# Kernel tuning notes

Measured on AMD Instinct MI355X. Metric: run time of the kernel, lower is better.

The kernel has to match this reference:

```python
import jax, jax.numpy as jnp
import numpy as np

R_HEADS = 4   # read heads
CELL = 64     # cell_size (word width)
MEM = 512     # nr_cells
DELTA = 1e-6


def _content_weights(mem, keys, strengths):
    # mem: (B,M,Wc), keys: (B,K,Wc), strengths: (B,K) -> (B,K,M)
    mn = jnp.linalg.norm(mem, axis=2, keepdims=True) + DELTA
    kn = jnp.linalg.norm(keys, axis=2, keepdims=True) + DELTA
    d = jnp.einsum('bkw,bmw->bkm', keys / kn, mem / mn)  # cosine similarity
    return jax.nn.softmax(d * strengths[:, :, None], axis=2)


def _allocate(usage):
    # usage: (B,M) -> allocation weighting (B,M)
    B = usage.shape[0]
    u = DELTA + (1.0 - DELTA) * usage
    idx = jnp.argsort(u, axis=1)                               # ascending usage
    sorted_u = jnp.take_along_axis(u, idx, axis=1)
    prod_su = jnp.cumprod(
        jnp.concatenate([jnp.ones((B, 1), u.dtype), sorted_u], axis=1), axis=1)[:, :-1]
    sorted_alloc = (1.0 - sorted_u) * prod_su
    inv = jnp.argsort(idx, axis=1)                             # inverse permutation
    return jnp.take_along_axis(sorted_alloc, inv, axis=1)


def dnc_forward(x, W_ih, b_ih, W_hh, b_hh, W_out, b_out, W_int, b_int, W_mem, b_mem):
    B, T, IN = x.shape
    H = W_hh.shape[1]
    r, w, m = R_HEADS, CELL, MEM
    eye_mask = 1.0 - jnp.eye(m, dtype=x.dtype)  # zero link-matrix diagonal

    def step(carry, x_t):
        h, c, mem, link, prec, read_w, write_w, usage, last_read = carry
        # controller LSTM cell (torch gate order i,f,g,o)
        inp = jnp.concatenate([x_t, last_read], axis=1)
        gates = inp @ W_ih.T + b_ih + h @ W_hh.T + b_hh
        gi, gf, gg, go = jnp.split(gates, 4, axis=1)
        c = jax.nn.sigmoid(gf) * c + jax.nn.sigmoid(gi) * jnp.tanh(gg)
        h = jax.nn.sigmoid(go) * jnp.tanh(c)
        out = h @ W_out.T + b_out
        xi = h @ W_int.T + b_int  # interface vector, size r*w+3w+5r+3
        # parse interface
        o = r * w
        read_keys = jnp.tanh(xi[:, :r * w].reshape(B, r, w))
        read_str = jax.nn.softplus(xi[:, o:o + r]); o += r
        write_key = jnp.tanh(xi[:, o:o + w].reshape(B, 1, w)); o += w
        write_str = jax.nn.softplus(xi[:, o:o + 1]); o += 1
        erase = jax.nn.sigmoid(xi[:, o:o + w].reshape(B, 1, w)); o += w
        write_vec = jnp.tanh(xi[:, o:o + w].reshape(B, 1, w)); o += w
        free_gates = jax.nn.sigmoid(xi[:, o:o + r]); o += r
        alloc_gate = jax.nn.sigmoid(xi[:, o:o + 1]); o += 1
        write_gate = jax.nn.sigmoid(xi[:, o:o + 1]); o += 1
        read_modes = jax.nn.softmax(xi[:, o:o + 3 * r].reshape(B, r, 3), axis=-1)

        # ---- write ----
        usage = usage + (1 - usage) * (1 - jnp.prod(1 - write_w, axis=1))
        psi = jnp.prod(1 - free_gates[:, :, None] * read_w, axis=1)
        usage = usage * psi
        wcw = _content_weights(mem, write_key, write_str)      # (B,1,M)
        alloc = _allocate(usage)[:, None, :]                   # (B,1,M)
        ag = alloc_gate[:, :, None]
        write_w = write_gate[:, :, None] * (ag * alloc + (1 - ag) * wcw)
        reset = jnp.prod(1 - write_w[:, :, :, None] * erase[:, :, None, :], axis=1)  # (B,M,Wc)
        mem = mem * reset + jnp.einsum('bkm,bkw->bmw', write_w, write_vec)
        ww = write_w[:, 0]                                     # (B,M), single write head
        L = link[:, 0]
        L = (1 - ww[:, :, None] - ww[:, None, :]) * L + ww[:, :, None] * prec[:, 0][:, None, :]
        L = L * eye_mask
        link = L[:, None]
        prec = (1 - jnp.sum(write_w, axis=2, keepdims=True)) * prec + write_w

        # ---- read ----
        cw = _content_weights(mem, read_keys, read_str)        # (B,R,M)
        fwd = jnp.einsum('bij,brj->bri', L, read_w)
        bwd = jnp.einsum('bri,bij->brj', read_w, L)
        read_w = (read_modes[:, :, 0:1] * bwd
                  + read_modes[:, :, 1:2] * fwd
                  + read_modes[:, :, 2:3] * cw)
        read_vecs = jnp.einsum('brm,bmw->brw', read_w, mem).reshape(B, r * w)
        y = jnp.concatenate([out, read_vecs], axis=1) @ W_mem.T + b_mem
        return (h, c, mem, link, prec, read_w, write_w, usage, read_vecs), y

    z = lambda *s: jnp.zeros(s, x.dtype)
    carry0 = (z(B, H), z(B, H), z(B, m, w), z(B, 1, m, m), z(B, 1, m),
              z(B, r, m), z(B, 1, m), z(B, m), z(B, r * w))
    _, ys = jax.lax.scan(step, carry0, jnp.swapaxes(x, 0, 1))
    return jnp.swapaxes(ys, 0, 1)  # (B,T,IN)


def setup_inputs() -> dict:
    key = jax.random.key(0)
    ks = jax.random.split(key, 12)
    B, T, IN, H = 16, 32, 256, 512
    r, w = R_HEADS, CELL
    iface = w * r + 3 * w + 5 * r + 3  # 471
    s = 0.05
    return {
        'x': jax.random.normal(ks[0], (B, T, IN), jnp.float32),
        'W_ih': jax.random.normal(ks[1], (4 * H, IN + r * w), jnp.float32) * s,
        'b_ih': jax.random.normal(ks[2], (4 * H,), jnp.float32) * s,
        'W_hh': jax.random.normal(ks[3], (4 * H, H), jnp.float32) * s,
        'b_hh': jax.random.normal(ks[4], (4 * H,), jnp.float32) * s,
        'W_out': jax.random.normal(ks[5], (H, H), jnp.float32) * s,
        'b_out': jax.random.normal(ks[6], (H,), jnp.float32) * s,
        'W_int': jax.random.normal(ks[7], (iface, H), jnp.float32) * s,
        'b_int': jax.random.normal(ks[8], (iface,), jnp.float32) * s,
        'W_mem': jax.random.normal(ks[9], (IN, r * w + H), jnp.float32) * s,
        'b_mem': jax.random.normal(ks[10], (IN,), jnp.float32) * s,
    }


def reference(x, W_ih, b_ih, W_hh, b_hh, W_out, b_out, W_int, b_int, W_mem, b_mem):
    return dnc_forward(x, W_ih, b_ih, W_hh, b_hh, W_out, b_out, W_int, b_int, W_mem, b_mem)
```

## Files before the change

### kernel.cpp

```cpp
#include <hip/hip_runtime.h>
#include <math.h>

#define NB 16
#define NT 256
#define NWG 256
#define TT 32
#define INP 256
#define HH 512
#define RH 4
#define CWID 64
#define MM 512
#define IFACE 471
#define DELTA 1e-6f
#define AP 516

__device__ __align__(16) float g_h[2][NB][HH];
__device__ __align__(16) float g_c[NB][HH];
__device__ __align__(16) float g_lr[NB][INP];
__device__ __align__(16) float g_usage[NB][MM];
__device__ __align__(16) float g_ww[NB][MM];
__device__ __align__(16) float g_prec[2][NB][MM];
__device__ __align__(16) float g_rw[NB][RH][MM];
__device__ __align__(16) float g_mem[NB][MM][CWID];
__device__ __align__(16) float g_L[NB][MM][MM];
__device__ __align__(16) float g_out[NB][HH];
__device__ __align__(16) float g_xi[NB][HH];
__device__ __align__(16) float g_rkn[NB][RH][CWID];
__device__ __align__(16) float g_rs[NB][RH];
__device__ __align__(16) float g_erase[NB][CWID];
__device__ __align__(16) float g_wv[NB][CWID];
__device__ __align__(16) float g_modes[NB][RH][3];
__device__ __align__(16) float g_fwd[NB][RH][MM];
__device__ __align__(16) float g_bwdp[NB][16][RH][MM];
__device__ __align__(16) float g_e[NB][RH][MM];
__device__ __align__(16) float g_cwsp[NB][16][RH];
__device__ __align__(16) float g_rvp[NB][16][RH][CWID];

struct P {
  const float *x, *W_ih, *b_ih, *W_hh, *b_hh, *W_out, *b_out, *W_int, *b_int, *W_mem, *b_mem;
  float* y;
};

__device__ __forceinline__ float sigf(float x)  { return 1.f / (1.f + __expf(-x)); }
__device__ __forceinline__ float splus(float x) { return fmaxf(x, 0.f) + log1pf(__expf(-fabsf(x))); }

__device__ __forceinline__ void zfill(float* a, long n) {
  const long stride = (long)gridDim.x * blockDim.x;
  for (long i = (long)blockIdx.x * blockDim.x + threadIdx.x; i < n; i += stride) a[i] = 0.f;
}

__global__ void __launch_bounds__(NT) k_init() {
  zfill(&g_h[0][0][0], 2L*NB*HH);
  zfill(&g_c[0][0], (long)NB*HH);
  zfill(&g_lr[0][0], (long)NB*INP);
  zfill(&g_usage[0][0], (long)NB*MM);
  zfill(&g_ww[0][0], (long)NB*MM);
  zfill(&g_prec[0][0][0], 2L*NB*MM);
  zfill(&g_rw[0][0][0], (long)NB*RH*MM);
  zfill(&g_mem[0][0][0], (long)NB*MM*CWID);
  zfill(&g_L[0][0][0], (long)NB*MM*MM);
}

__global__ void __launch_bounds__(NT) k_ph1(P p, int t) {
  __shared__ __align__(16) float sm[14432];
  float* As  = sm;
  float* Ws  = sm + 16*AP;
  float* red = sm + 24*AP;
  const int tid = threadIdx.x;
  const int j0  = 2 * (int)blockIdx.x;
  const int op  = tid & 3;
  const int bq  = (tid >> 2) & 3;
  const int ks  = tid >> 4;
  const float (*hsrc)[HH] = g_h[t & 1];
  float acc0[4] = {0.f,0.f,0.f,0.f};
  float acc1[4] = {0.f,0.f,0.f,0.f};
  for (int pass = 0; pass < 2; ++pass) {
    if (pass == 0) {
      for (int idx = tid; idx < NB*INP; idx += NT) {
        int b = idx >> 8, k = idx & 255;
        As[b*AP + k] = p.x[((size_t)b*TT + t)*INP + k];
      }
      for (int idx = tid; idx < NB*INP; idx += NT) {
        int b = idx >> 8, k = idx & 255;
        As[b*AP + INP + k] = g_lr[b][k];
      }
    } else {
      for (int idx = tid; idx < NB*HH; idx += NT) {
        int b = idx >> 9, k = idx & 511;
        As[b*AP + k] = hsrc[b][k];
      }
    }
    const float* Wsrc = pass ? p.W_hh : p.W_ih;
    for (int idx = tid; idx < 8*512; idx += NT) {
      int ro = idx >> 9, k = idx & 511;
      int row = (ro >> 1)*HH + j0 + (ro & 1);
      Ws[ro*AP + k] = Wsrc[(size_t)row*512 + k];
    }
    __syncthreads();
    const int k0 = ks * 32;
    #pragma unroll
    for (int k4 = 0; k4 < 32; k4 += 4) {
      const float4 w0 = *(const float4*)&Ws[(op*2+0)*AP + k0 + k4];
      const float4 w1 = *(const float4*)&Ws[(op*2+1)*AP + k0 + k4];
      #pragma unroll
      for (int bb = 0; bb < 4; ++bb) {
        const float4 a = *(const float4*)&As[(bq*4+bb)*AP + k0 + k4];
        acc0[bb] += a.x*w0.x + a.y*w0.y + a.z*w0.z + a.w*w0.w;
        acc1[bb] += a.x*w1.x + a.y*w1.y + a.z*w1.z + a.w*w1.w;
      }
    }
    __syncthreads();
  }
  #pragma unroll
  for (int bb = 0; bb < 4; ++bb) {
    red[(op*2+0)*256 + (bq*4+bb)*16 + ks] = acc0[bb];
    red[(op*2+1)*256 + (bq*4+bb)*16 + ks] = acc1[bb];
  }
  __syncthreads();
  if (tid < 128) {
    int o = tid >> 4, b = tid & 15;
    float s = 0.f;
    #pragma unroll
    for (int q = 0; q < 16; ++q) s += red[o*256 + b*16 + q];
    int row = (o >> 1)*HH + j0 + (o & 1);
    red[o*256 + b*16] = s + p.b_ih[row] + p.b_hh[row];
  }
  __syncthreads();
  if (tid < 32) {
    int jj = tid >> 4, b = tid & 15;
    int j  = j0 + jj;
    float gi = red[(0+jj)*256 + b*16];
    float gf = red[(2+jj)*256 + b*16];
    float gg = red[(4+jj)*256 + b*16];
    float go = red[(6+jj)*256 + b*16];
    float c0 = g_c[b][j];
    float cn = sigf(gf)*c0 + sigf(gi)*tanhf(gg);
    float hn = sigf(go)*tanhf(cn);
    g_c[b][j] = cn;
    g_h[(t+1) & 1][b][j] = hn;
  }
}

__global__ void __launch_bounds__(NT) k_ph2(P p, int t) {
  __shared__ __align__(16) float sm[10576];
  float* hs  = sm;
  float* Ws  = sm + 16*AP;
  float* red = sm + 20*AP;
  const int tid = threadIdx.x;
  const int o0  = 4 * (int)blockIdx.x;
  const float (*hcur)[HH] = g_h[(t+1) & 1];
  for (int idx = tid; idx < NB*HH; idx += NT) {
    int b = idx >> 9, k = idx & 511;
    hs[b*AP + k] = hcur[b][k];
  }
  for (int idx = tid; idx < 4*512; idx += NT) {
    int oi = idx >> 9, k = idx & 511;
    int o = o0 + oi;
    float v = 0.f;
    if (o < HH)              v = p.W_out[(size_t)o*512 + k];
    else if (o < HH + IFACE) v = p.W_int[(size_t)(o - HH)*512 + k];
    Ws[oi*AP + k] = v;
  }
  __syncthreads();
  {
    const int b = tid & 15, oi = (tid >> 4) & 3, ks = tid >> 6;
    const int k0 = ks * 128;
    float acc = 0.f;
    #pragma unroll 8
    for (int k4 = 0; k4 < 128; k4 += 4) {
      const float4 a  = *(const float4*)&hs[b*AP + k0 + k4];
      const float4 wv = *(const float4*)&Ws[oi*AP + k0 + k4];
      acc += a.x*wv.x + a.y*wv.y + a.z*wv.z + a.w*wv.w;
    }
    red[(oi*16 + b)*4 + ks] = acc;
  }
  __syncthreads();
  if (tid < 64) {
    int oi = tid >> 4, b = tid & 15;
    int base = (oi*16 + b)*4;
    float s = red[base] + red[base+1] + red[base+2] + red[base+3];
    int o = o0 + oi;
    if (o < HH) g_out[b][o] = s + p.b_out[o];
    else if (o < HH + IFACE) g_xi[b][o - HH] = s + p.b_int[o - HH];
  }
}

__global__ void __launch_bounds__(512) k_ph3(int pp) {
  __shared__ __align__(16) float sm[4152];
  const int b = (int)blockIdx.x, tid = threadIdx.x;
  float* xi_l = sm;
  float* wkn  = sm + 472;
  float* sc   = sm + 536;
  float* u_l  = sm + 552;
  float* wcw  = sm + 1064;
  float* su   = sm + 1576;
  float* cB   = sm + 2600;
  float* wwl  = sm + 3112;
  float* red  = sm + 3624;
  int*   rnk  = (int*)(sm + 3640);

  for (int i = tid; i < IFACE; i += 512) xi_l[i] = g_xi[b][i];
  __syncthreads();
  {
    const int wv = tid >> 6, v = tid & 63;
    if (wv < 4) {
      float kv = tanhf(xi_l[wv*64 + v]);
      float ss = kv * kv;
      #pragma unroll
      for (int d = 1; d < 64; d <<= 1) ss += __shfl_xor(ss, d, 64);
      g_rkn[b][wv][v] = kv / (sqrtf(ss) + DELTA);
      if (v == 0) { float s_ = splus(xi_l[256 + wv]); sc[wv] = s_; g_rs[b][wv] = s_; }
    } else if (wv == 4) {
      float kv = tanhf(xi_l[260 + v]);
      float ss = kv * kv;
      #pragma unroll
      for (int d = 1; d < 64; d <<= 1) ss += __shfl_xor(ss, d, 64);
      wkn[v] = kv / (sqrtf(ss) + DELTA);
    } else if (wv == 5) {
      g_erase[b][v] = sigf(xi_l[325 + v]);
    } else if (wv == 6) {
      g_wv[b][v] = tanhf(xi_l[389 + v]);
    } else {
      if (v < 4)       sc[4 + v] = sigf(xi_l[453 + v]);
      else if (v == 4) sc[8] = sigf(xi_l[457]);
      else if (v == 5) sc[9] = sigf(xi_l[458]);
      else if (v == 6) sc[10] = splus(xi_l[324]);
      else if (v >= 8 && v < 12) {
        int r = v - 8;
        float a0 = xi_l[459 + r*3], a1 = xi_l[459 + r*3 + 1], a2 = xi_l[459 + r*3 + 2];
        float mx = fmaxf(a0, fmaxf(a1, a2));
        float e0 = __expf(a0 - mx), e1 = __expf(a1 - mx), e2 = __expf(a2 - mx);
        float si = e0 + e1 + e2;
        g_modes[b][r][0] = e0/si; g_modes[b][r][1] = e1/si; g_modes[b][r][2] = e2/si;
      }
    }
  }
  __syncthreads();
  {
    float uo = g_usage[b][tid];
    float wwp = g_ww[b][tid];
    float psi = 1.f;
    #pragma unroll
    for (int r = 0; r < RH; ++r) psi *= 1.f - sc[4+r]*g_rw[b][r][tid];
    float un = (uo + (1.f - uo)*wwp) * psi;
    g_usage[b][tid] = un;
    u_l[tid] = DELTA + (1.f - DELTA)*un;
  }
  {
    float dot = 0.f, nn = 0.f;
    const float* mr = &g_mem[b][tid][0];
    #pragma unroll
    for (int v4 = 0; v4 < CWID; v4 += 4) {
      float4 m4 = *(const float4*)&mr[v4];
      dot += m4.x*wkn[v4] + m4.y*wkn[v4+1] + m4.z*wkn[v4+2] + m4.w*wkn[v4+3];
      nn  += m4.x*m4.x + m4.y*m4.y + m4.z*m4.z + m4.w*m4.w;
    }
    wcw[tid] = (dot / (sqrtf(nn) + DELTA)) * sc[10];
  }
  __syncthreads();
  {
    const int wv = tid >> 6, v = tid & 63;
    float x0 = wcw[tid];
    float mx = x0;
    #pragma unroll
    for (int d = 1; d < 64; d <<= 1) mx = fmaxf(mx, __shfl_xor(mx, d, 64));
    if (v == 0) red[wv] = mx;
    __syncthreads();
    float gmx = red[0];
    #pragma unroll
    for (int q = 1; q < 8; ++q) gmx = fmaxf(gmx, red[q]);
    float e0 = __expf(x0 - gmx);
    float ss = e0;
    #pragma unroll
    for (int d = 1; d < 64; d <<= 1) ss += __shfl_xor(ss, d, 64);
    if (v == 0) red[8 + wv] = ss;
    __syncthreads();
    float tot = red[8];
    #pragma unroll
    for (int q = 9; q < 16; ++q) tot += red[q];
    wcw[tid] = e0 / tot;
  }
  __syncthreads();
  {
    const float u0 = u_l[tid];
    int cnt = 0;
    for (int j = 0; j < MM; j += 8) {
      const float4 a = *(const float4*)&u_l[j];
      const float4 c = *(const float4*)&u_l[j + 4];
      cnt += (a.x < u0) || (a.x == u0 && (j+0) < tid);
      cnt += (a.y < u0) || (a.y == u0 && (j+1) < tid);
      cnt += (a.z < u0) || (a.z == u0 && (j+2) < tid);
      cnt += (a.w < u0) || (a.w == u0 && (j+3) < tid);
      cnt += (c.x < u0) || (c.x == u0 && (j+4) < tid);
      cnt += (c.y < u0) || (c.y == u0 && (j+5) < tid);
      cnt += (c.z < u0) || (c.z == u0 && (j+6) < tid);
      cnt += (c.w < u0) || (c.w == u0 && (j+7) < tid);
    }
    rnk[tid] = cnt;
    su[cnt] = u0;
  }
  __syncthreads();
  {
    const int lane = tid & 63, wv = tid >> 6;
    float v = su[tid];
    #pragma unroll
    for (int d = 1; d < 64; d <<= 1) {
      float m = __shfl_up(v, d, 64);
      if (lane >= d) v *= m;
    }
    if (lane == 63) red[wv] = v;
    __syncthreads();
    float pre = 1.f;
    for (int q = 0; q < wv; ++q) pre *= red[q];
    cB[tid] = v * pre;
    __syncthreads();
    float ag = sc[8], wgt = sc[9];
    int rk = rnk[tid];
    float excl = rk ? cB[rk - 1] : 1.f;
    float alloc = (1.f - u_l[tid]) * excl;
    float wn = wgt * (ag*alloc + (1.f - ag)*wcw[tid]);
    wwl[tid] = wn;
    g_ww[b][tid] = wn;
  }
  __syncthreads();
  {
    const int wv = tid >> 6, v = tid & 63;
    float s2 = wwl[tid];
    #pragma unroll
    for (int d = 1; d < 64; d <<= 1) s2 += __shfl_xor(s2, d, 64);
    if (v == 0) red[wv] = s2;
    __syncthreads();
    float sww = red[0];
    #pragma unroll
    for (int q = 1; q < 8; ++q) sww += red[q];
    g_prec[1 - pp][b][tid] = (1.f - sww)*g_prec[pp][b][tid] + wwl[tid];
  }
}

__global__ void __launch_bounds__(NT) k_ph4(int pp) {
  __shared__ __align__(16) float sm[6608];
  const int w = (int)blockIdx.x, tid = threadIdx.x;
  const int b = w >> 4, s = w & 15, i0 = s * 32;
  float* pl   = sm;
  float* wwl  = sm + 512;
  float* rwl  = sm + 1024;
  float* el   = sm + 3072;
  float* wvl  = sm + 3136;
  float* rknl = sm + 3200;
  float* rs4  = sm + 3456;
  float* fp   = sm + 3472;
  float* mt   = sm + 4496;
  float* nrm  = sm + 6576;

  for (int i = tid; i < MM; i += NT) { pl[i] = g_prec[pp][b][i]; wwl[i] = g_ww[b][i]; }
  for (int i = tid; i < RH*MM; i += NT) rwl[i] = g_rw[b][i >> 9][i & 511];
  for (int i = tid; i < CWID; i += NT) { el[i] = g_erase[b][i]; wvl[i] = g_wv[b][i]; }
  for (int i = tid; i < RH*CWID; i += NT) rknl[i] = g_rkn[b][i >> 6][i & 63];
  if (tid < 4) rs4[tid] = g_rs[b][tid];
  __syncthreads();
  {
    const int ii = tid >> 3, js = tid & 7;
    const int i = i0 + ii;
    const float wwi = wwl[i];
    float f0=0.f, f1=0.f, f2=0.f, f3=0.f;
    float* Lrow = &g_L[b][i][0];
    #pragma unroll
    for (int step = 0; step < 16; ++step) {
      const int col = js*64 + ((js*8 + step*4) & 63);
      float4 l4 = *(float4*)&Lrow[col];
      float lv[4] = {l4.x, l4.y, l4.z, l4.w};
      #pragma unroll
      for (int q = 0; q < 4; ++q) {
        const int jq = col + q;
        float lnv = (1.f - wwi - wwl[jq]) * lv[q] + wwi * pl[jq];
        if (jq == i) lnv = 0.f;
        lv[q] = lnv;
        f0 += lnv * rwl[jq];
        f1 += lnv * rwl[512 + jq];
        f2 += lnv * rwl[1024 + jq];
        f3 += lnv * rwl[1536 + jq];
      }
      *(float4*)&Lrow[col] = make_float4(lv[0], lv[1], lv[2], lv[3]);
    }
    fp[(ii*8 + js)*4 + 0] = f0;
    fp[(ii*8 + js)*4 + 1] = f1;
    fp[(ii*8 + js)*4 + 2] = f2;
    fp[(ii*8 + js)*4 + 3] = f3;
  }
  __syncthreads();
  if (tid < 128) {
    int ii = tid >> 2, r = tid & 3;
    float sY = 0.f;
    #pragma unroll
    for (int js = 0; js < 8; ++js) sY += fp[(ii*8 + js)*4 + r];
    g_fwd[b][r][i0 + ii] = sY;
  }
  {
    const int j = tid * 2;
    float a00=0,a01=0,a10=0,a11=0,a20=0,a21=0,a30=0,a31=0;
    #pragma unroll 4
    for (int ii2 = 0; ii2 < 32; ++ii2) {
      const int i = i0 + ii2;
      const float2 l2 = *(const float2*)&g_L[b][i][j];
      const float r0 = rwl[i], r1 = rwl[512+i], r2 = rwl[1024+i], r3 = rwl[1536+i];
      a00 += r0*l2.x; a01 += r0*l2.y;
      a10 += r1*l2.x; a11 += r1*l2.y;
      a20 += r2*l2.x; a21 += r2*l2.y;
      a30 += r3*l2.x; a31 += r3*l2.y;
    }
    g_bwdp[b][s][0][j] = a00; g_bwdp[b][s][0][j+1] = a01;
    g_bwdp[b][s][1][j] = a10; g_bwdp[b][s][1][j+1] = a11;
    g_bwdp[b][s][2][j] = a20; g_bwdp[b][s][2][j+1] = a21;
    g_bwdp[b][s][3][j] = a30; g_bwdp[b][s][3][j+1] = a31;
  }
  for (int idx = tid; idx < 32*CWID; idx += NT) {
    int ii = idx >> 6, v = idx & 63;
    int i = i0 + ii;
    float wwi = wwl[i];
    float mv = g_mem[b][i][v];
    float mn = mv * (1.f - wwi*el[v]) + wwi*wvl[v];
    g_mem[b][i][v] = mn;
    mt[ii*65 + v] = mn;
  }
  __syncthreads();
  {
    int ii = tid >> 3, js = tid & 7;
    float nn = 0.f;
    #pragma unroll
    for (int q = 0; q < 8; ++q) { float mv = mt[ii*65 + js*8 + q]; nn += mv*mv; }
    fp[(ii*8 + js)*4] = nn;
  }
  __syncthreads();
  if (tid < 32) {
    float nn = 0.f;
    #pragma unroll
    for (int q = 0; q < 8; ++q) nn += fp[(tid*8 + q)*4];
    nrm[tid] = sqrtf(nn) + DELTA;
  }
  __syncthreads();
  {
    int ii = tid >> 3, js = tid & 7;
    float p0=0,p1=0,p2=0,p3=0;
    #pragma unroll
    for (int q = 0; q < 8; ++q) {
      float mv = mt[ii*65 + js*8 + q];
      p0 += mv * rknl[ 0 + js*8 + q];
      p1 += mv * rknl[ 64 + js*8 + q];
      p2 += mv * rknl[128 + js*8 + q];
      p3 += mv * rknl[192 + js*8 + q];
    }
    fp[(ii*8 + js)*4 + 0] = p0;
    fp[(ii*8 + js)*4 + 1] = p1;
    fp[(ii*8 + js)*4 + 2] = p2;
    fp[(ii*8 + js)*4 + 3] = p3;
  }
  __syncthreads();
  if (tid < 128) {
    int ii = tid >> 2, r = tid & 3;
    float d = 0.f;
    #pragma unroll
    for (int js = 0; js < 8; ++js) d += fp[(ii*8 + js)*4 + r];
    float e = __expf((d / nrm[ii]) * rs4[r]);
    g_e[b][r][i0 + ii] = e;
    mt[ii*4 + r] = e;
  }
  __syncthreads();
  if (tid < 4) {
    float ssum = 0.f;
    #pragma unroll
    for (int q = 0; q < 32; ++q) ssum += mt[q*4 + tid];
    g_cwsp[b][s][tid] = ssum;
  }
}

__global__ void __launch_bounds__(NT) k_ph5() {
  __shared__ __align__(16) float sm[144];
  const int w = (int)blockIdx.x, tid = threadIdx.x;
  const int b = w >> 4, s = w & 15, j0 = s * 32;
  float* Sr  = sm;
  float* rwt = sm + 16;
  if (tid < 4) {
    float ss = 0.f;
    #pragma unroll
    for (int q = 0; q < 16; ++q) ss += g_cwsp[b][q][tid];
    Sr[tid] = ss;
  }
  __syncthreads();
  if (tid < 128) {
    int jj = tid >> 2, r = tid & 3;
    int j = j0 + jj;
    float bw = 0.f;
    #pragma unroll
    for (int q = 0; q < 16; ++q) bw += g_bwdp[b][q][r][j];
    float fw = g_fwd[b][r][j];
    float cwv = g_e[b][r][j] / Sr[r];
    float rn = g_modes[b][r][0]*bw + g_modes[b][r][1]*fw + g_modes[b][r][2]*cwv;
    g_rw[b][r][j] = rn;
    rwt[r*32 + jj] = rn;
  }
  __syncthreads();
  {
    int r = tid >> 6, v = tid & 63;
    float acc = 0.f;
    #pragma unroll
    for (int jj = 0; jj < 32; ++jj) acc += rwt[r*32 + jj] * g_mem[b][j0 + jj][v];
    g_rvp[b][s][r][v] = acc;
  }
}

__global__ void __launch_bounds__(NT) k_ph6(P p, int t) {
  __shared__ __align__(16) float sm[1024];
  const int w = (int)blockIdx.x, tid = threadIdx.x;
  const int b = w >> 4, s = w & 15, o0 = s * 16;
  float* rv   = sm;
  float* outl = sm + 256;
  float* red  = sm + 768;
  {
    int r = tid >> 6, v = tid & 63;
    float acc = 0.f;
    #pragma unroll
    for (int q = 0; q < 16; ++q) acc += g_rvp[b][q][r][v];
    rv[r*64 + v] = acc;
    if (s == 0) g_lr[b][r*64 + v] = acc;
  }
  for (int k = tid; k < HH; k += NT) outl[k] = g_out[b][k];
  __syncthreads();
  {
    int oi = tid & 15, ks = tid >> 4;
    int o = o0 + oi;
    const float* wm = &p.W_mem[(size_t)o * 768];
    float acc = 0.f;
    for (int k = ks*48; k < ks*48 + 48; ++k) {
      float a = (k < HH) ? outl[k] : rv[k - HH];
      acc += a * wm[k];
    }
    red[oi*16 + ks] = acc;
  }
  __syncthreads();
  if (tid < 16) {
    int o = o0 + tid;
    float ss = 0.f;
    #pragma unroll
    for (int q = 0; q < 16; ++q) ss += red[tid*16 + q];
    p.y[((size_t)b*TT + t)*INP + o] = ss + p.b_mem[o];
  }
}

extern "C" void kernel_launch(void* const* d_in, const int* in_sizes, int n_in,
                              void* d_out, int out_size, void* d_ws, size_t ws_size,
                              hipStream_t stream) {
  (void)in_sizes; (void)n_in; (void)out_size; (void)d_ws; (void)ws_size;
  P p;
  p.x     = (const float*)d_in[0];
  p.W_ih  = (const float*)d_in[1];
  p.b_ih  = (const float*)d_in[2];
  p.W_hh  = (const float*)d_in[3];
  p.b_hh  = (const float*)d_in[4];
  p.W_out = (const float*)d_in[5];
  p.b_out = (const float*)d_in[6];
  p.W_int = (const float*)d_in[7];
  p.b_int = (const float*)d_in[8];
  p.W_mem = (const float*)d_in[9];
  p.b_mem = (const float*)d_in[10];
  p.y     = (float*)d_out;

  k_init<<<dim3(1024), dim3(NT), 0, stream>>>();
  for (int t = 0; t < TT; ++t) {
    const int pp = t & 1;
    k_ph1<<<dim3(NWG), dim3(NT), 0, stream>>>(p, t);
    k_ph2<<<dim3(NWG), dim3(NT), 0, stream>>>(p, t);
    k_ph3<<<dim3(NB),  dim3(512), 0, stream>>>(pp);
    k_ph4<<<dim3(NWG), dim3(NT), 0, stream>>>(pp);
    k_ph5<<<dim3(NWG), dim3(NT), 0, stream>>>();
    k_ph6<<<dim3(NWG), dim3(NT), 0, stream>>>(p, t);
  }
}
```

Measured before the change: 2.162 ms.

## Hoist output projections out of the recurrent loop into batched post-loop kernels

The output projection (W_out on h) and the final y projection (W_mem on out and read vectors) are not on the recurrence path, so they move out of the per-timestep loop. Hidden states and per-slice read-vector partials are stored for every timestep, and two kernels run after the loop to compute all outputs at once, with weights held in shared memory. This removes one kernel launch per step and shrinks the ph2 grid to only the interface rows. In exchange it costs extra global buffers, and ph1 now sums the 16 read-vector partials itself.

```diff
diff --git a/kernel.cpp b/kernel.cpp
--- a/kernel.cpp
+++ b/kernel.cpp
@@ -13,17 +13,16 @@
 #define IFACE 471
 #define DELTA 1e-6f
 #define AP 516
+#define WMP 772
 
 __device__ __align__(16) float g_h[2][NB][HH];
 __device__ __align__(16) float g_c[NB][HH];
-__device__ __align__(16) float g_lr[NB][INP];
 __device__ __align__(16) float g_usage[NB][MM];
 __device__ __align__(16) float g_ww[NB][MM];
 __device__ __align__(16) float g_prec[2][NB][MM];
 __device__ __align__(16) float g_rw[NB][RH][MM];
 __device__ __align__(16) float g_mem[NB][MM][CWID];
 __device__ __align__(16) float g_L[NB][MM][MM];
-__device__ __align__(16) float g_out[NB][HH];
 __device__ __align__(16) float g_xi[NB][HH];
 __device__ __align__(16) float g_rkn[NB][RH][CWID];
 __device__ __align__(16) float g_rs[NB][RH];
@@ -34,7 +33,9 @@
 __device__ __align__(16) float g_bwdp[NB][16][RH][MM];
 __device__ __align__(16) float g_e[NB][RH][MM];
 __device__ __align__(16) float g_cwsp[NB][16][RH];
-__device__ __align__(16) float g_rvp[NB][16][RH][CWID];
+__device__ __align__(16) float g_hs[NB][TT][HH];
+__device__ __align__(16) float g_outs[NB][TT][HH];
+__device__ __align__(16) float g_rvps[NB][TT][16][RH*CWID];
 
 struct P {
   const float *x, *W_ih, *b_ih, *W_hh, *b_hh, *W_out, *b_out, *W_int, *b_int, *W_mem, *b_mem;
@@ -52,7 +53,6 @@
 __global__ void __launch_bounds__(NT) k_init() {
   zfill(&g_h[0][0][0], 2L*NB*HH);
   zfill(&g_c[0][0], (long)NB*HH);
-  zfill(&g_lr[0][0], (long)NB*INP);
   zfill(&g_usage[0][0], (long)NB*MM);
   zfill(&g_ww[0][0], (long)NB*MM);
   zfill(&g_prec[0][0][0], 2L*NB*MM);
@@ -82,7 +82,13 @@
       }
       for (int idx = tid; idx < NB*INP; idx += NT) {
         int b = idx >> 8, k = idx & 255;
-        As[b*AP + INP + k] = g_lr[b][k];
+        float s = 0.f;
+        if (t > 0) {
+          const float* rp = &g_rvps[b][t-1][0][k];
+          #pragma unroll
+          for (int q = 0; q < 16; ++q) s += rp[q*(RH*CWID)];
+        }
+        As[b*AP + INP + k] = s;
       }
     } else {
       for (int idx = tid; idx < NB*HH; idx += NT) {
@@ -138,6 +144,7 @@
     float hn = sigf(go)*tanhf(cn);
     g_c[b][j] = cn;
     g_h[(t+1) & 1][b][j] = hn;
+    g_hs[b][t][j] = hn;
   }
 }
 
@@ -156,10 +163,7 @@
   for (int idx = tid; idx < 4*512; idx += NT) {
     int oi = idx >> 9, k = idx & 511;
     int o = o0 + oi;
-    float v = 0.f;
-    if (o < HH)              v = p.W_out[(size_t)o*512 + k];
-    else if (o < HH + IFACE) v = p.W_int[(size_t)(o - HH)*512 + k];
-    Ws[oi*AP + k] = v;
+    Ws[oi*AP + k] = (o < IFACE) ? p.W_int[(size_t)o*512 + k] : 0.f;
   }
   __syncthreads();
   {
@@ -180,8 +184,7 @@
     int base = (oi*16 + b)*4;
     float s = red[base] + red[base+1] + red[base+2] + red[base+3];
     int o = o0 + oi;
-    if (o < HH) g_out[b][o] = s + p.b_out[o];
-    else if (o < HH + IFACE) g_xi[b][o - HH] = s + p.b_int[o - HH];
+    if (o < IFACE) g_xi[b][o] = s + p.b_int[o];
   }
 }
 
@@ -473,7 +476,7 @@
   }
 }
 
-__global__ void __launch_bounds__(NT) k_ph5() {
+__global__ void __launch_bounds__(NT) k_ph5(int t) {
   __shared__ __align__(16) float sm[144];
   const int w = (int)blockIdx.x, tid = threadIdx.x;
   const int b = w >> 4, s = w & 15, j0 = s * 32;
@@ -504,45 +507,92 @@
     float acc = 0.f;
     #pragma unroll
     for (int jj = 0; jj < 32; ++jj) acc += rwt[r*32 + jj] * g_mem[b][j0 + jj][v];
-    g_rvp[b][s][r][v] = acc;
-  }
-}
-
-__global__ void __launch_bounds__(NT) k_ph6(P p, int t) {
-  __shared__ __align__(16) float sm[1024];
+    g_rvps[b][t][s][tid] = acc;
+  }
+}
+
+__global__ void __launch_bounds__(NT) k_out_all(P p) {
+  __shared__ __align__(16) float sm[10576];
+  float* hs  = sm;
+  float* Ws  = sm + 16*AP;
+  float* red = sm + 20*AP;
+  const int tid = threadIdx.x;
+  const int wg  = (int)blockIdx.x & 127;
+  const int tg  = (int)blockIdx.x >> 7;
+  const int o0  = 4 * wg;
+  for (int idx = tid; idx < 4*512; idx += NT) {
+    int oi = idx >> 9, k = idx & 511;
+    Ws[oi*AP + k] = p.W_out[(size_t)(o0 + oi)*512 + k];
+  }
+  for (int tt = 0; tt < 16; ++tt) {
+    const int t = tg*16 + tt;
+    __syncthreads();
+    for (int idx = tid; idx < NB*HH; idx += NT) {
+      int b = idx >> 9, k = idx & 511;
+      hs[b*AP + k] = g_hs[b][t][k];
+    }
+    __syncthreads();
+    {
+      const int b = tid & 15, oi = (tid >> 4) & 3, ks = tid >> 6;
+      const int k0 = ks * 128;
+      float acc = 0.f;
+      #pragma unroll 8
+      for (int k4 = 0; k4 < 128; k4 += 4) {
+        const float4 a  = *(const float4*)&hs[b*AP + k0 + k4];
+        const float4 wv = *(const float4*)&Ws[oi*AP + k0 + k4];
+        acc += a.x*wv.x + a.y*wv.y + a.z*wv.z + a.w*wv.w;
+      }
+      red[(oi*16 + b)*4 + ks] = acc;
+    }
+    __syncthreads();
+    if (tid < 64) {
+      int oi = tid >> 4, b = tid & 15;
+      int base = (oi*16 + b)*4;
+      float s = red[base] + red[base+1] + red[base+2] + red[base+3];
+      g_outs[b][t][o0 + oi] = s + p.b_out[o0 + oi];
+    }
+  }
+}
+
+__global__ void __launch_bounds__(NT) k_y_all(P p) {
+  __shared__ __align__(16) float sm[16*WMP + 1024];
+  float* Wm   = sm;
+  float* outl = sm + 16*WMP;
+  float* rv   = sm + 16*WMP+512;
+  float* red  = sm + 16*WMP+768;
   const int w = (int)blockIdx.x, tid = threadIdx.x;
   const int b = w >> 4, s = w & 15, o0 = s * 16;
-  float* rv   = sm;
-  float* outl = sm + 256;
-  float* red  = sm + 768;
-  {
-    int r = tid >> 6, v = tid & 63;
-    float acc = 0.f;
-    #pragma unroll
-    for (int q = 0; q < 16; ++q) acc += g_rvp[b][q][r][v];
-    rv[r*64 + v] = acc;
-    if (s == 0) g_lr[b][r*64 + v] = acc;
-  }
-  for (int k = tid; k < HH; k += NT) outl[k] = g_out[b][k];
-  __syncthreads();
-  {
-    int oi = tid & 15, ks = tid >> 4;
-    int o = o0 + oi;
-    const float* wm = &p.W_mem[(size_t)o * 768];
-    float acc = 0.f;
-    for (int k = ks*48; k < ks*48 + 48; ++k) {
-      float a = (k < HH) ? outl[k] : rv[k - HH];
-      acc += a * wm[k];
-    }
-    red[oi*16 + ks] = acc;
-  }
-  __syncthreads();
-  if (tid < 16) {
-    int o = o0 + tid;
-    float ss = 0.f;
-    #pragma unroll
-    for (int q = 0; q < 16; ++q) ss += red[tid*16 + q];
-    p.y[((size_t)b*TT + t)*INP + o] = ss + p.b_mem[o];
+  for (int row = 0; row < 16; ++row)
+    for (int k = tid; k < 768; k += NT)
+      Wm[row*WMP + k] = p.W_mem[(size_t)(o0 + row)*768 + k];
+  for (int t = 0; t < TT; ++t) {
+    __syncthreads();
+    for (int k = tid; k < HH; k += NT) outl[k] = g_outs[b][t][k];
+    {
+      float acc = 0.f;
+      const float* rp = &g_rvps[b][t][0][tid];
+      #pragma unroll
+      for (int q = 0; q < 16; ++q) acc += rp[q*(RH*CWID)];
+      rv[tid] = acc;
+    }
+    __syncthreads();
+    {
+      int oi = tid & 15, ks = tid >> 4;
+      const float* wm = &Wm[oi*WMP];
+      float acc = 0.f;
+      for (int k = ks*48; k < ks*48 + 48; ++k) {
+        float a = (k < HH) ? outl[k] : rv[k - HH];
+        acc += a * wm[k];
+      }
+      red[oi*16 + ks] = acc;
+    }
+    __syncthreads();
+    if (tid < 16) {
+      float ss = 0.f;
+      #pragma unroll
+      for (int q = 0; q < 16; ++q) ss += red[tid*16 + q];
+      p.y[((size_t)b*TT + t)*INP + o0 + tid] = ss + p.b_mem[o0 + tid];
+    }
   }
 }
 
@@ -568,10 +618,11 @@
   for (int t = 0; t < TT; ++t) {
     const int pp = t & 1;
     k_ph1<<<dim3(NWG), dim3(NT), 0, stream>>>(p, t);
-    k_ph2<<<dim3(NWG), dim3(NT), 0, stream>>>(p, t);
+    k_ph2<<<dim3(118), dim3(NT), 0, stream>>>(p, t);
     k_ph3<<<dim3(NB),  dim3(512), 0, stream>>>(pp);
     k_ph4<<<dim3(NWG), dim3(NT), 0, stream>>>(pp);
-    k_ph5<<<dim3(NWG), dim3(NT), 0, stream>>>();
-    k_ph6<<<dim3(NWG), dim3(NT), 0, stream>>>(p, t);
-  }
-}
+    k_ph5<<<dim3(NWG), dim3(NT), 0, stream>>>(t);
+  }
+  k_out_all<<<dim3(256), dim3(NT), 0, stream>>>(p);
+  k_y_all<<<dim3(256), dim3(NT), 0, stream>>>(p);
+}
```

Result: slower. 2.304 ms (+6.6%).

## Move output projection off critical path into ph5 and skip link-matrix zero fill

Applied to the files above, without the earlier changes.

Phase 2 now computes only the interface vector (118 blocks instead of 256), and the W_out output projection moves into phase 5, where it runs beside the read-vector work. The aim is to shorten the serial chain leading into the memory-update phases. Separately, the 16 MB zero fill of the link matrix in init is removed, and phase 4 treats L as zero on the first timestep. In exchange, phase 5 takes on extra global weight reads per block and more shared memory.

```diff
diff --git a/kernel.cpp b/kernel.cpp
--- a/kernel.cpp
+++ b/kernel.cpp
@@ -58,7 +58,6 @@
   zfill(&g_prec[0][0][0], 2L*NB*MM);
   zfill(&g_rw[0][0][0], (long)NB*RH*MM);
   zfill(&g_mem[0][0][0], (long)NB*MM*CWID);
-  zfill(&g_L[0][0][0], (long)NB*MM*MM);
 }
 
 __global__ void __launch_bounds__(NT) k_ph1(P p, int t) {
@@ -156,10 +155,7 @@
   for (int idx = tid; idx < 4*512; idx += NT) {
     int oi = idx >> 9, k = idx & 511;
     int o = o0 + oi;
-    float v = 0.f;
-    if (o < HH)              v = p.W_out[(size_t)o*512 + k];
-    else if (o < HH + IFACE) v = p.W_int[(size_t)(o - HH)*512 + k];
-    Ws[oi*AP + k] = v;
+    Ws[oi*AP + k] = (o < IFACE) ? p.W_int[(size_t)o*512 + k] : 0.f;
   }
   __syncthreads();
   {
@@ -180,8 +176,7 @@
     int base = (oi*16 + b)*4;
     float s = red[base] + red[base+1] + red[base+2] + red[base+3];
     int o = o0 + oi;
-    if (o < HH) g_out[b][o] = s + p.b_out[o];
-    else if (o < HH + IFACE) g_xi[b][o - HH] = s + p.b_int[o - HH];
+    if (o < IFACE) g_xi[b][o] = s + p.b_int[o];
   }
 }
 
@@ -337,7 +332,7 @@
   }
 }
 
-__global__ void __launch_bounds__(NT) k_ph4(int pp) {
+__global__ void __launch_bounds__(NT) k_ph4(int pp, int zeroL) {
   __shared__ __align__(16) float sm[6608];
   const int w = (int)blockIdx.x, tid = threadIdx.x;
   const int b = w >> 4, s = w & 15, i0 = s * 32;
@@ -367,7 +362,7 @@
     #pragma unroll
     for (int step = 0; step < 16; ++step) {
       const int col = js*64 + ((js*8 + step*4) & 63);
-      float4 l4 = *(float4*)&Lrow[col];
+      float4 l4 = zeroL ? make_float4(0.f,0.f,0.f,0.f) : *(float4*)&Lrow[col];
       float lv[4] = {l4.x, l4.y, l4.z, l4.w};
       #pragma unroll
       for (int q = 0; q < 4; ++q) {
@@ -473,12 +468,16 @@
   }
 }
 
-__global__ void __launch_bounds__(NT) k_ph5() {
-  __shared__ __align__(16) float sm[144];
+__global__ void __launch_bounds__(NT) k_ph5(P p, int t) {
+  __shared__ __align__(16) float sm[960];
+  float* Sr   = sm;
+  float* rwt  = sm + 16;
+  float* red2 = sm + 144;
+  float* hl   = sm + 400;
   const int w = (int)blockIdx.x, tid = threadIdx.x;
-  const int b = w >> 4, s = w & 15, j0 = s * 32;
-  float* Sr  = sm;
-  float* rwt = sm + 16;
+  const int b = w >> 4, s = w & 15, j0 = s * 32, o0 = s * 32;
+  const float (*hcur)[HH] = g_h[(t+1) & 1];
+  for (int k = tid; k < HH; k += NT) hl[k + ((k >> 6) << 2)] = hcur[b][k];
   if (tid < 4) {
     float ss = 0.f;
     #pragma unroll
@@ -505,6 +504,25 @@
     #pragma unroll
     for (int jj = 0; jj < 32; ++jj) acc += rwt[r*32 + jj] * g_mem[b][j0 + jj][v];
     g_rvp[b][s][r][v] = acc;
+  }
+  {
+    int oi = tid >> 3, ks = tid & 7;
+    const float* wrow = &p.W_out[(size_t)(o0 + oi)*512 + ks*64];
+    const float* hk   = &hl[ks*68];
+    float acc = 0.f;
+    #pragma unroll
+    for (int i = 0; i < 64; i += 4) {
+      const float4 wv = *(const float4*)&wrow[i];
+      acc += hk[i]*wv.x + hk[i+1]*wv.y + hk[i+2]*wv.z + hk[i+3]*wv.w;
+    }
+    red2[oi*8 + ks] = acc;
+  }
+  __syncthreads();
+  if (tid < 32) {
+    float ssum = 0.f;
+    #pragma unroll
+    for (int q = 0; q < 8; ++q) ssum += red2[tid*8 + q];
+    g_out[b][o0 + tid] = ssum + p.b_out[o0 + tid];
   }
 }
 
@@ -568,10 +586,10 @@
   for (int t = 0; t < TT; ++t) {
     const int pp = t & 1;
     k_ph1<<<dim3(NWG), dim3(NT), 0, stream>>>(p, t);
-    k_ph2<<<dim3(NWG), dim3(NT), 0, stream>>>(p, t);
+    k_ph2<<<dim3(118), dim3(NT), 0, stream>>>(p, t);
     k_ph3<<<dim3(NB),  dim3(512), 0, stream>>>(pp);
-    k_ph4<<<dim3(NWG), dim3(NT), 0, stream>>>(pp);
-    k_ph5<<<dim3(NWG), dim3(NT), 0, stream>>>();
+    k_ph4<<<dim3(NWG), dim3(NT), 0, stream>>>(pp, t == 0 ? 1 : 0);
+    k_ph5<<<dim3(NWG), dim3(NT), 0, stream>>>(p, t);
     k_ph6<<<dim3(NWG), dim3(NT), 0, stream>>>(p, t);
   }
 }
```

Measured after the change: 2.276 ms. 5.3% more time.

## Fuse read-weight and output-projection phases into one per-batch kernel

Applied to the files above, without the earlier changes.

Merges k_ph5 and k_ph6 into a single kernel with one 512-thread workgroup per batch element. The read vectors now stay in shared memory instead of going through the g_rvp partial buffer, and one launch per timestep is removed. The trade-off is that only 16 workgroups run instead of 256, so each does longer serial loops: 256-long over memory rows and 384-long over W_mem. That cuts parallelism across the GPU and may leave most CUs idle.

```diff
diff --git a/kernel.cpp b/kernel.cpp
--- a/kernel.cpp
+++ b/kernel.cpp
@@ -34,7 +34,6 @@
 __device__ __align__(16) float g_bwdp[NB][16][RH][MM];
 __device__ __align__(16) float g_e[NB][RH][MM];
 __device__ __align__(16) float g_cwsp[NB][16][RH];
-__device__ __align__(16) float g_rvp[NB][16][RH][CWID];
 
 struct P {
   const float *x, *W_ih, *b_ih, *W_hh, *b_hh, *W_out, *b_out, *W_int, *b_int, *W_mem, *b_mem;
@@ -473,77 +472,68 @@
   }
 }
 
-__global__ void __launch_bounds__(NT) k_ph5() {
-  __shared__ __align__(16) float sm[144];
-  const int w = (int)blockIdx.x, tid = threadIdx.x;
-  const int b = w >> 4, s = w & 15, j0 = s * 32;
-  float* Sr  = sm;
-  float* rwt = sm + 16;
+__global__ void __launch_bounds__(512) k_ph56(P p, int t) {
+  __shared__ __align__(16) float sm[3856];
+  float* rwl  = sm;
+  float* outl = sm + 2048;
+  float* rvh  = sm + 2560;
+  float* rvl  = sm + 3072;
+  float* red  = sm + 3328;
+  float* Sr   = sm + 3840;
+  const int b = (int)blockIdx.x, tid = threadIdx.x;
   if (tid < 4) {
     float ss = 0.f;
     #pragma unroll
     for (int q = 0; q < 16; ++q) ss += g_cwsp[b][q][tid];
     Sr[tid] = ss;
   }
-  __syncthreads();
-  if (tid < 128) {
-    int jj = tid >> 2, r = tid & 3;
-    int j = j0 + jj;
-    float bw = 0.f;
-    #pragma unroll
-    for (int q = 0; q < 16; ++q) bw += g_bwdp[b][q][r][j];
-    float fw = g_fwd[b][r][j];
-    float cwv = g_e[b][r][j] / Sr[r];
-    float rn = g_modes[b][r][0]*bw + g_modes[b][r][1]*fw + g_modes[b][r][2]*cwv;
-    g_rw[b][r][j] = rn;
-    rwt[r*32 + jj] = rn;
-  }
-  __syncthreads();
-  {
-    int r = tid >> 6, v = tid & 63;
+  for (int k = tid; k < HH; k += 512) outl[k] = g_out[b][k];
+  __syncthreads();
+  {
+    const int j = tid;
+    #pragma unroll
+    for (int r = 0; r < RH; ++r) {
+      float bw = 0.f;
+      #pragma unroll
+      for (int q = 0; q < 16; ++q) bw += g_bwdp[b][q][r][j];
+      float fw = g_fwd[b][r][j];
+      float cwv = g_e[b][r][j] / Sr[r];
+      float rn = g_modes[b][r][0]*bw + g_modes[b][r][1]*fw + g_modes[b][r][2]*cwv;
+      g_rw[b][r][j] = rn;
+      rwl[r*512 + j] = rn;
+    }
+  }
+  __syncthreads();
+  {
+    const int half = tid >> 8, rv_i = tid & 255;
+    const int r = rv_i >> 6, v = rv_i & 63;
+    const int j0 = half * 256;
     float acc = 0.f;
-    #pragma unroll
-    for (int jj = 0; jj < 32; ++jj) acc += rwt[r*32 + jj] * g_mem[b][j0 + jj][v];
-    g_rvp[b][s][r][v] = acc;
-  }
-}
-
-__global__ void __launch_bounds__(NT) k_ph6(P p, int t) {
-  __shared__ __align__(16) float sm[1024];
-  const int w = (int)blockIdx.x, tid = threadIdx.x;
-  const int b = w >> 4, s = w & 15, o0 = s * 16;
-  float* rv   = sm;
-  float* outl = sm + 256;
-  float* red  = sm + 768;
-  {
-    int r = tid >> 6, v = tid & 63;
+    for (int jj = 0; jj < 256; ++jj)
+      acc += rwl[r*512 + j0 + jj] * g_mem[b][j0 + jj][v];
+    rvh[half*256 + rv_i] = acc;
+  }
+  __syncthreads();
+  if (tid < 256) {
+    float rv = rvh[tid] + rvh[256 + tid];
+    rvl[tid] = rv;
+    g_lr[b][tid] = rv;
+  }
+  __syncthreads();
+  {
+    const int oi = tid >> 1, half = tid & 1;
+    const float* wm = &p.W_mem[(size_t)oi * 768 + half*384];
     float acc = 0.f;
-    #pragma unroll
-    for (int q = 0; q < 16; ++q) acc += g_rvp[b][q][r][v];
-    rv[r*64 + v] = acc;
-    if (s == 0) g_lr[b][r*64 + v] = acc;
-  }
-  for (int k = tid; k < HH; k += NT) outl[k] = g_out[b][k];
-  __syncthreads();
-  {
-    int oi = tid & 15, ks = tid >> 4;
-    int o = o0 + oi;
-    const float* wm = &p.W_mem[(size_t)o * 768];
-    float acc = 0.f;
-    for (int k = ks*48; k < ks*48 + 48; ++k) {
-      float a = (k < HH) ? outl[k] : rv[k - HH];
+    for (int k = 0; k < 384; ++k) {
+      int kk = half*384 + k;
+      float a = (kk < HH) ? outl[kk] : rvl[kk - HH];
       acc += a * wm[k];
     }
-    red[oi*16 + ks] = acc;
-  }
-  __syncthreads();
-  if (tid < 16) {
-    int o = o0 + tid;
-    float ss = 0.f;
-    #pragma unroll
-    for (int q = 0; q < 16; ++q) ss += red[tid*16 + q];
-    p.y[((size_t)b*TT + t)*INP + o] = ss + p.b_mem[o];
-  }
+    red[oi*2 + half] = acc;
+  }
+  __syncthreads();
+  if (tid < 256)
+    p.y[((size_t)b*TT + t)*INP + tid] = red[tid*2] + red[tid*2 + 1] + p.b_mem[tid];
 }
 
 extern "C" void kernel_launch(void* const* d_in, const int* in_sizes, int n_in,
@@ -571,7 +561,6 @@
     k_ph2<<<dim3(NWG), dim3(NT), 0, stream>>>(p, t);
     k_ph3<<<dim3(NB),  dim3(512), 0, stream>>>(pp);
     k_ph4<<<dim3(NWG), dim3(NT), 0, stream>>>(pp);
-    k_ph5<<<dim3(NWG), dim3(NT), 0, stream>>>();
-    k_ph6<<<dim3(NWG), dim3(NT), 0, stream>>>(p, t);
-  }
-}
+    k_ph56<<<dim3(NB), dim3(512), 0, stream>>>(p, t);
+  }
+}
```

Measured after the change: 3.099 ms. 1.43x slower.
